# Performance work log

Hardware: AMD Instinct MI355X
Metric: run time of the kernel (lower is better)

The kernel has to match this reference:

```python
import jax, jax.numpy as jnp
import numpy as np

WEIGHT = 1.0
EPS = 1e-12  # matches torch F.normalize eps


def setup_inputs() -> dict:
    key = jax.random.key(0)
    k1, k2 = jax.random.split(key)
    B, N, D = 32, 4096, 512
    x = jax.random.normal(k1, (B, N, D), dtype=jnp.float32)
    ref = jax.random.normal(k2, (B, N, D), dtype=jnp.float32)
    return {"x": x, "ref": ref}


def _l2norm(t, axis):
    # torch.nn.functional.normalize: t / max(||t||_2, eps)
    n = jnp.sqrt(jnp.sum(t * t, axis=axis, keepdims=True))
    return t / jnp.maximum(n, EPS)


def reference(x, ref):
    B, N, D = x.shape
    # trace(A @ B^T) == sum(A * B); fused normalize + elementwise + reduce, O(N*D)
    # row-normalized term (dim=1 in torch == last axis per row)
    a_per = jnp.sum(_l2norm(x, 2) * _l2norm(ref, 2), axis=(1, 2)) / N * WEIGHT  # [B]
    # column-normalized term (dim=0 in torch == axis 1 here)
    b_per = jnp.sum(_l2norm(x, 1) * _l2norm(ref, 1), axis=(1, 2)) / D * WEIGHT  # [B]
    a = -jnp.sum(a_per) / B
    b = -jnp.sum(b_per) / B
    return a + b
```

## Files before the change

kernel.cpp:

```cpp
#include <hip/hip_runtime.h>
#include <math.h>


#define BB 32
#define NN 4096
#define DD 512

static constexpr float EPS = 1e-12f;
static constexpr int BPB   = 64;
static constexpr int RPB   = NN / BPB;
static constexpr int NWAVE = 4;
static constexpr int RPW   = RPB / NWAVE;
static constexpr int SUB   = 4;
static constexpr int NSUB  = RPW / SUB;

static constexpr size_t WS_CXX = 0;
static constexpr size_t WS_CRR = (size_t)BB * DD;
static constexpr size_t WS_CXR = (size_t)2 * BB * DD;
static constexpr size_t WS_ROW = (size_t)3 * BB * DD;
static constexpr size_t WS_FLOATS = WS_ROW + 1;

__global__ __launch_bounds__(256, 4) void spl_pass1(
    const float* __restrict__ x, const float* __restrict__ r, float* __restrict__ ws) {
  __shared__ float lds[NWAVE][3][DD / 2];
  __shared__ float ldsrow[NWAVE];

  const int tid  = threadIdx.x;
  const int wave = tid >> 6;
  const int lane = tid & 63;
  const int blk  = blockIdx.x;
  const int b    = blk / BPB;
  const int bib  = blk % BPB;
  const int n0   = bib * RPB + wave * RPW;

  float cxx[8], crr[8], cxr[8];
#pragma unroll
  for (int j = 0; j < 8; ++j) { cxx[j] = 0.f; crr[j] = 0.f; cxr[j] = 0.f; }
  float rowacc = 0.f;

  const size_t base = (size_t)b * NN * DD + (size_t)n0 * DD;
  const float* xb = x + base;
  const float* rb = r + base;

#pragma unroll 1
  for (int s = 0; s < NSUB; ++s) {
    float4 xd[SUB][2], rd[SUB][2];
#pragma unroll
    for (int rr = 0; rr < SUB; ++rr) {
      const float4* xp = (const float4*)(xb + (size_t)(s * SUB + rr) * DD);
      const float4* rp = (const float4*)(rb + (size_t)(s * SUB + rr) * DD);
      xd[rr][0] = xp[lane];
      xd[rr][1] = xp[lane + 64];
      rd[rr][0] = rp[lane];
      rd[rr][1] = rp[lane + 64];
    }

    float sxx[SUB], srr[SUB], sxr[SUB];
#pragma unroll
    for (int rr = 0; rr < SUB; ++rr) {
      sxx[rr] = 0.f; srr[rr] = 0.f; sxr[rr] = 0.f;
#pragma unroll
      for (int k = 0; k < 2; ++k) {
        const float xs[4] = {xd[rr][k].x, xd[rr][k].y, xd[rr][k].z, xd[rr][k].w};
        const float rs[4] = {rd[rr][k].x, rd[rr][k].y, rd[rr][k].z, rd[rr][k].w};
#pragma unroll
        for (int j = 0; j < 4; ++j) {
          const float pxx = xs[j] * xs[j];
          const float prr = rs[j] * rs[j];
          const float pxr = xs[j] * rs[j];
          sxx[rr] += pxx; srr[rr] += prr; sxr[rr] += pxr;
          cxx[k * 4 + j] += pxx; crr[k * 4 + j] += prr; cxr[k * 4 + j] += pxr;
        }
      }
    }

#pragma unroll
    for (int off = 1; off < 64; off <<= 1) {
#pragma unroll
      for (int rr = 0; rr < SUB; ++rr) {
        sxx[rr] += __shfl_xor(sxx[rr], off, 64);
        srr[rr] += __shfl_xor(srr[rr], off, 64);
        sxr[rr] += __shfl_xor(sxr[rr], off, 64);
      }
    }
#pragma unroll
    for (int rr = 0; rr < SUB; ++rr) {
      const float nx = fmaxf(sqrtf(sxx[rr]), EPS);
      const float nr = fmaxf(sqrtf(srr[rr]), EPS);
      rowacc += sxr[rr] / (nx * nr);
    }
  }

  if (lane == 0) ldsrow[wave] = rowacc;

  __syncthreads();
  {
    float4* cb = (float4*)&lds[0][0][0];
#pragma unroll
    for (int m = 0; m < 3; ++m) {
      const float* c = (m == 0) ? cxx : (m == 1) ? crr : cxr;
      cb[(wave * 3 + m) * 64 + lane] = make_float4(c[0], c[1], c[2], c[3]);
    }
  }
  __syncthreads();
  for (int i = tid; i < 768; i += 256) {
    const int m = i >> 8;
    const int d = i & 255;
    const float sum = lds[0][m][d] + lds[1][m][d] + lds[2][m][d] + lds[3][m][d];
    atomicAdd(ws + (size_t)m * BB * DD + (size_t)b * DD + d, sum);
  }

  __syncthreads();
  {
    float4* cb = (float4*)&lds[0][0][0];
#pragma unroll
    for (int m = 0; m < 3; ++m) {
      const float* c = (m == 0) ? cxx : (m == 1) ? crr : cxr;
      cb[(wave * 3 + m) * 64 + lane] = make_float4(c[4], c[5], c[6], c[7]);
    }
  }
  __syncthreads();
  for (int i = tid; i < 768; i += 256) {
    const int m = i >> 8;
    const int d = i & 255;
    const float sum = lds[0][m][d] + lds[1][m][d] + lds[2][m][d] + lds[3][m][d];
    atomicAdd(ws + (size_t)m * BB * DD + (size_t)b * DD + 256 + d, sum);
  }

  if (tid == 0) {
    atomicAdd(ws + WS_ROW, ldsrow[0] + ldsrow[1] + ldsrow[2] + ldsrow[3]);
  }
}

__global__ __launch_bounds__(256) void spl_pass2(const float* __restrict__ ws,
                                                 float* __restrict__ out) {
  const int tid = threadIdx.x;
  const float* cxx_g = ws + WS_CXX;
  const float* crr_g = ws + WS_CRR;
  const float* cxr_g = ws + WS_CXR;

  float acc = 0.f;
  for (int i = tid; i < BB * DD; i += 256) {
    const float sxx = cxx_g[i];
    const float srr = crr_g[i];
    const float sxr = cxr_g[i];
    const float nx = fmaxf(sqrtf(sxx), EPS);
    const float nr = fmaxf(sqrtf(srr), EPS);
    acc += sxr / (nx * nr);
  }
#pragma unroll
  for (int off = 1; off < 64; off <<= 1) acc += __shfl_xor(acc, off, 64);

  __shared__ float wsum[4];
  if ((tid & 63) == 0) wsum[tid >> 6] = acc;
  __syncthreads();
  if (tid == 0) {
    const float colsum = wsum[0] + wsum[1] + wsum[2] + wsum[3];
    const float rowsum = ws[WS_ROW];
    const float a = -rowsum / ((float)NN * (float)BB);
    const float b = -colsum / ((float)DD * (float)BB);
    out[0] = a + b;
  }
}

extern "C" void kernel_launch(void* const* d_in, const int* in_sizes, int n_in,
                              void* d_out, int out_size, void* d_ws, size_t ws_size,
                              hipStream_t stream) {
  const float* x = (const float*)d_in[0];
  const float* r = (const float*)d_in[1];
  float* out = (float*)d_out;
  float* ws = (float*)d_ws;

  (void)in_sizes; (void)n_in; (void)out_size; (void)ws_size;

  hipMemsetAsync(ws, 0, WS_FLOATS * sizeof(float), stream);
  spl_pass1<<<BB * BPB, 256, 0, stream>>>(x, r, ws);
  spl_pass2<<<1, 256, 0, stream>>>(ws, out);
}
```

Measured before the change: 146.8 us.

## Replace global atomics with per-block partials and a two-stage parallel reduction

Pass 1 now writes each block's column partial sums and row term into its own workspace slot instead of issuing atomicAdds into shared accumulators. A new 256-block pass 2 reduces the 64 partials per batch and feature slice, and a one-block pass 3 combines the results. This removes atomic contention, the memset, and the serial single-block column reduction. In exchange it adds an extra kernel launch and about 13 MB of partial-sum traffic.

```diff
diff --git a/kernel.cpp b/kernel.cpp
--- a/kernel.cpp
+++ b/kernel.cpp
@@ -14,11 +14,9 @@
 static constexpr int SUB   = 4;
 static constexpr int NSUB  = RPW / SUB;
 
-static constexpr size_t WS_CXX = 0;
-static constexpr size_t WS_CRR = (size_t)BB * DD;
-static constexpr size_t WS_CXR = (size_t)2 * BB * DD;
-static constexpr size_t WS_ROW = (size_t)3 * BB * DD;
-static constexpr size_t WS_FLOATS = WS_ROW + 1;
+static constexpr size_t S1     = 1600;
+static constexpr size_t WS_W2  = (size_t)2048 * S1;
+static constexpr size_t WS_FLOATS = WS_W2 + 256;
 
 __global__ __launch_bounds__(256, 4) void spl_pass1(
     const float* __restrict__ x, const float* __restrict__ r, float* __restrict__ ws) {
@@ -93,6 +91,8 @@
 
   if (lane == 0) ldsrow[wave] = rowacc;
 
+  float* P = ws + (size_t)blk * S1;
+
   __syncthreads();
   {
     float4* cb = (float4*)&lds[0][0][0];
@@ -106,8 +106,7 @@
   for (int i = tid; i < 768; i += 256) {
     const int m = i >> 8;
     const int d = i & 255;
-    const float sum = lds[0][m][d] + lds[1][m][d] + lds[2][m][d] + lds[3][m][d];
-    atomicAdd(ws + (size_t)m * BB * DD + (size_t)b * DD + d, sum);
+    P[m * 512 + d] = lds[0][m][d] + lds[1][m][d] + lds[2][m][d] + lds[3][m][d];
   }
 
   __syncthreads();
@@ -123,31 +122,51 @@
   for (int i = tid; i < 768; i += 256) {
     const int m = i >> 8;
     const int d = i & 255;
-    const float sum = lds[0][m][d] + lds[1][m][d] + lds[2][m][d] + lds[3][m][d];
-    atomicAdd(ws + (size_t)m * BB * DD + (size_t)b * DD + 256 + d, sum);
+    P[m * 512 + 256 + d] = lds[0][m][d] + lds[1][m][d] + lds[2][m][d] + lds[3][m][d];
   }
 
   if (tid == 0) {
-    atomicAdd(ws + WS_ROW, ldsrow[0] + ldsrow[1] + ldsrow[2] + ldsrow[3]);
+    P[1536] = ldsrow[0] + ldsrow[1] + ldsrow[2] + ldsrow[3];
   }
 }
 
-__global__ __launch_bounds__(256) void spl_pass2(const float* __restrict__ ws,
+__global__ __launch_bounds__(64, 8) void spl_pass2(const float* __restrict__ ws,
+                                                   float* __restrict__ ws2) {
+  const int lane = threadIdx.x;
+  const int g    = blockIdx.x;
+  const int b    = g >> 3;
+  const int d    = (g & 7) * 64 + lane;
+
+  float sxx = 0.f, srr = 0.f, sxr = 0.f;
+  const float* Pb = ws + (size_t)(b * BPB) * S1;
+#pragma unroll 4
+  for (int bib = 0; bib < BPB; ++bib) {
+    const float* P = Pb + (size_t)bib * S1;
+    sxx += P[d];
+    srr += P[512 + d];
+    sxr += P[1024 + d];
+  }
+  const float nx = fmaxf(sqrtf(sxx), EPS);
+  const float nr = fmaxf(sqrtf(srr), EPS);
+  float term = sxr / (nx * nr);
+#pragma unroll
+  for (int off = 1; off < 64; off <<= 1) term += __shfl_xor(term, off, 64);
+
+  float rterm = 0.f;
+  if ((g & 7) == 0) {
+    float rv = Pb[(size_t)lane * S1 + 1536];
+#pragma unroll
+    for (int off = 1; off < 64; off <<= 1) rv += __shfl_xor(rv, off, 64);
+    rterm = rv / (float)NN;
+  }
+
+  if (lane == 0) ws2[g] = term / (float)DD + rterm;
+}
+
+__global__ __launch_bounds__(256) void spl_pass3(const float* __restrict__ ws2,
                                                  float* __restrict__ out) {
   const int tid = threadIdx.x;
-  const float* cxx_g = ws + WS_CXX;
-  const float* crr_g = ws + WS_CRR;
-  const float* cxr_g = ws + WS_CXR;
-
-  float acc = 0.f;
-  for (int i = tid; i < BB * DD; i += 256) {
-    const float sxx = cxx_g[i];
-    const float srr = crr_g[i];
-    const float sxr = cxr_g[i];
-    const float nx = fmaxf(sqrtf(sxx), EPS);
-    const float nr = fmaxf(sqrtf(srr), EPS);
-    acc += sxr / (nx * nr);
-  }
+  float acc = ws2[tid];
 #pragma unroll
   for (int off = 1; off < 64; off <<= 1) acc += __shfl_xor(acc, off, 64);
 
@@ -155,11 +174,7 @@
   if ((tid & 63) == 0) wsum[tid >> 6] = acc;
   __syncthreads();
   if (tid == 0) {
-    const float colsum = wsum[0] + wsum[1] + wsum[2] + wsum[3];
-    const float rowsum = ws[WS_ROW];
-    const float a = -rowsum / ((float)NN * (float)BB);
-    const float b = -colsum / ((float)DD * (float)BB);
-    out[0] = a + b;
+    out[0] = -(wsum[0] + wsum[1] + wsum[2] + wsum[3]) / (float)BB;
   }
 }
 
@@ -173,7 +188,7 @@
 
   (void)in_sizes; (void)n_in; (void)out_size; (void)ws_size;
 
-  hipMemsetAsync(ws, 0, WS_FLOATS * sizeof(float), stream);
   spl_pass1<<<BB * BPB, 256, 0, stream>>>(x, r, ws);
-  spl_pass2<<<1, 256, 0, stream>>>(ws, out);
+  spl_pass2<<<256, 64, 0, stream>>>(ws, ws + WS_W2);
+  spl_pass3<<<1, 256, 0, stream>>>(ws + WS_W2, out);
 }
```

New measurement: 122.9 us, median of 2. 16.3% less time.
